# Optimization experiments

Measured on AMD Instinct MI355X. Metric: run time of the kernel, lower is better.

The kernel has to match this reference:

```python
import math
import jax, jax.numpy as jnp
import numpy as np

N_USERS = 100000
N_ITEMS = 50000
NNZ = 1600000
BATCH = 64
ORDER = 8
FLATNESS = 2


def cheby_coeffs(order, flatness):
    # plateau target on Chebyshev extrema grid
    x = np.arange(order + 1)
    xv = np.round(np.cos((order - x) / order * math.pi), 3)
    tgt = np.where(xv < 0,
                   np.power(-xv, flatness) * 0.5 + 0.5,
                   np.power(xv, flatness) * (-0.5) + 0.5)
    tgt = np.round(tgt, 3)
    # Chebyshev nodes
    k = np.arange(1, order + 2)
    nodes = np.cos((order + 1 + 0.5 - k) / (order + 1) * math.pi)
    # Chebyshev recurrence evaluated at nodes, scaled by target
    out = [tgt * np.ones_like(nodes) * 0 + tgt, nodes * tgt]
    for _ in range(2, order + 1):
        out.append(nodes * out[-1] * 2 - out[-2])
    c = np.stack(out).sum(axis=1) * (2.0 / (order + 1))
    c[0] /= 2
    return jnp.asarray(c, dtype=jnp.float32)


def setup_inputs() -> dict:
    key = jax.random.key(0)
    k1, k2, k3 = jax.random.split(key, 3)
    signal = jax.random.normal(k1, (BATCH, N_ITEMS), dtype=jnp.float32)
    row = jax.random.randint(k2, (NNZ,), 0, N_USERS)
    col = jax.random.randint(k3, (NNZ,), 0, N_ITEMS)
    # symmetric degree normalization D_u^{-1/2} A D_i^{-1/2}
    du = jnp.bincount(row, length=N_USERS).astype(jnp.float32)
    di = jnp.bincount(col, length=N_ITEMS).astype(jnp.float32)
    du_is = jnp.where(du > 0, jnp.clip(du, 1.0) ** -0.5, 0.0)
    di_is = jnp.where(di > 0, jnp.clip(di, 1.0) ** -0.5, 0.0)
    vals = du_is[row] * di_is[col]
    return {"signal": signal, "vals": vals, "row": row, "col": col}


def reference(signal, vals, row, col):
    coeffs = cheby_coeffs(ORDER, FLATNESS)

    def lap(x):  # x: [n_items, batch];  L*x = x - 2 * A^T (A x)
        y = jax.ops.segment_sum(vals[:, None] * x[col], row, num_segments=N_USERS)
        z = jax.ops.segment_sum(vals[:, None] * y[row], col, num_segments=N_ITEMS)
        return x - 2.0 * z

    s = signal.T  # [n_items, batch]
    t0 = s
    t1 = lap(s)
    out = coeffs[0] * t0 + coeffs[1] * t1
    for k in range(2, ORDER + 1):
        t2 = lap(t1) * 2.0 - t0
        out = out + coeffs[k] * t2
        t0, t1 = t1, t2
    return out.T
```

## Files before the change

### kernel.cpp

```cpp
#include <hip/hip_runtime.h>
#include <hip/hip_fp16.h>
#include <math.h>

#define NUSERS 100000
#define NITEMS 50000
#define BATCH  64
#define ORDER  8
#define BSHIFT 9
#define BROWS  (1 << BSHIFT)
#define NBUCKU ((NUSERS + BROWS - 1) >> BSHIFT)
#define NBUCKI ((NITEMS + BROWS - 1) >> BSHIFT)
#define CAPU 16384
#define CAPI 24576
#define S1_BLOCKS 512
#define NREP 4


struct __align__(8) Half4 { __half2 a, b; };
struct Coeffs { float v[ORDER + 1]; };

#define SLOT ((size_t)(NITEMS + 1) * BATCH)

__device__ __forceinline__ void acc_pk(float4& acc, Half4 v0, Half4 v1,
                                       Half4 v2, Half4 v3) {
    __half2 sa = __hadd2(__hadd2(v0.a, v1.a), __hadd2(v2.a, v3.a));
    __half2 sb = __hadd2(__hadd2(v0.b, v1.b), __hadd2(v2.b, v3.b));
    float2 fa = __half22float2(sa);
    float2 fb = __half22float2(sb);
    acc.x += fa.x; acc.y += fa.y; acc.z += fb.x; acc.w += fb.y;
}

__device__ __forceinline__ Half4 to_h4(float x, float y, float z, float w) {
    Half4 h;
    h.a = __floats2half2_rn(x, y);
    h.b = __floats2half2_rn(z, w);
    return h;
}

__global__ void init_bcur(int* __restrict__ bcurU, int* __restrict__ bcurI) {
    int t = blockIdx.x * blockDim.x + threadIdx.x;
    if (t < NBUCKU) bcurU[t] = t * CAPU;
    if (t < NBUCKI) bcurI[t] = t * CAPI;
}

__global__ void zero_pads(__half* __restrict__ tauHall, __half* __restrict__ ybuf) {
    int t = threadIdx.x;
    for (int k = 0; k <= ORDER; ++k)
        if (t < BATCH) tauHall[(size_t)k * SLOT + (size_t)NITEMS * BATCH + t] = __float2half(0.f);
    if (t < BATCH) ybuf[(size_t)NUSERS * BATCH + t] = __float2half(0.f);
}

__global__ void scatter1(const int* __restrict__ row, const int* __restrict__ col,
                         int* __restrict__ bcurU, int* __restrict__ bcurI,
                         int* __restrict__ stU, int* __restrict__ stI, int nnz) {
    __shared__ int cU[NREP][NBUCKU];
    __shared__ int cI[NREP][NBUCKI];
    const int chunk = (nnz + S1_BLOCKS - 1) / S1_BLOCKS;
    const int b0 = blockIdx.x * chunk;
    const int e0 = min(b0 + chunk, nnz);
    const int sw = threadIdx.x >> 6;
    for (int t = threadIdx.x; t < NREP * NBUCKU; t += blockDim.x) (&cU[0][0])[t] = 0;
    for (int t = threadIdx.x; t < NREP * NBUCKI; t += blockDim.x) (&cI[0][0])[t] = 0;
    __syncthreads();
    for (int i = b0 + threadIdx.x; i < e0; i += blockDim.x) {
        atomicAdd(&cU[sw][row[i] >> BSHIFT], 1);
        atomicAdd(&cI[sw][col[i] >> BSHIFT], 1);
    }
    __syncthreads();
    for (int t = threadIdx.x; t < NBUCKU; t += blockDim.x) {
        int c0 = cU[0][t], c1 = cU[1][t], c2 = cU[2][t], c3 = cU[3][t];
        int tot = c0 + c1 + c2 + c3;
        int base = (tot > 0) ? atomicAdd(&bcurU[t], tot) : 0;
        cU[0][t] = base;
        cU[1][t] = base + c0;
        cU[2][t] = base + c0 + c1;
        cU[3][t] = base + c0 + c1 + c2;
    }
    for (int t = threadIdx.x; t < NBUCKI; t += blockDim.x) {
        int c0 = cI[0][t], c1 = cI[1][t], c2 = cI[2][t], c3 = cI[3][t];
        int tot = c0 + c1 + c2 + c3;
        int base = (tot > 0) ? atomicAdd(&bcurI[t], tot) : 0;
        cI[0][t] = base;
        cI[1][t] = base + c0;
        cI[2][t] = base + c0 + c1;
        cI[3][t] = base + c0 + c1 + c2;
    }
    __syncthreads();
    for (int i = b0 + threadIdx.x; i < e0; i += blockDim.x) {
        int r = row[i], c = col[i];
        int pu = atomicAdd(&cU[sw][r >> BSHIFT], 1);
        stU[pu] = ((r & (BROWS - 1)) << 17) | c;
        int pi = atomicAdd(&cI[sw][c >> BSHIFT], 1);
        stI[pi] = ((c & (BROWS - 1)) << 17) | r;
    }
}

__global__ void scatter2(const int* __restrict__ bcur, const int* __restrict__ st,
                         int* __restrict__ ptr, int* __restrict__ degOut,
                         int* __restrict__ outIdx, int nrows, int cap, int dummyIdx) {
    __shared__ int deg[BROWS];
    __shared__ int ps[256];
    __shared__ int cur[BROWS];
    __shared__ int rs[BROWS];
    const int rbase = blockIdx.x << BSHIFT;
    const int nr = min(BROWS, nrows - rbase);
    const int lo = blockIdx.x * cap;
    const int hi = bcur[blockIdx.x];
    const int t = threadIdx.x;
    deg[2 * t] = 0;
    deg[2 * t + 1] = 0;
    __syncthreads();
    for (int j = lo + t; j < hi; j += 256)
        atomicAdd(&deg[st[j] >> 17], 1);
    __syncthreads();
    int a = deg[2 * t];
    int b = deg[2 * t + 1];
    int pa = (a + 15) & ~15;
    int pb = (b + 15) & ~15;
    ps[t] = pa + pb;
    __syncthreads();
    for (int off = 1; off < 256; off <<= 1) {
        int u = (t >= off) ? ps[t - off] : 0;
        __syncthreads();
        ps[t] += u;
        __syncthreads();
    }
    int excl = (t > 0) ? ps[t - 1] : 0;
    int p0 = lo + excl;
    int p1 = p0 + pa;
    rs[2 * t] = p0;
    rs[2 * t + 1] = p1;
    cur[2 * t] = p0;
    cur[2 * t + 1] = p1;
    if (2 * t < nr)     { ptr[rbase + 2 * t] = p0;     degOut[rbase + 2 * t] = a; }
    if (2 * t + 1 < nr) { ptr[rbase + 2 * t + 1] = p1; degOut[rbase + 2 * t + 1] = b; }
    __syncthreads();
    for (int j = lo + t; j < hi; j += 256) {
        int v = st[j];
        int p = atomicAdd(&cur[v >> 17], 1);
        outIdx[p] = v & 0x1FFFF;
    }
    __syncthreads();
    for (int i = t; i < nr; i += 256) {
        int endReal = cur[i];
        int endPad  = rs[i] + ((deg[i] + 15) & ~15);
        for (int j = endReal; j < endPad; ++j) outIdx[j] = dummyIdx;
    }
}

__global__ void transpose_scale_k(const float* __restrict__ in,
                                  const int* __restrict__ ideg,
                                  float* __restrict__ out,
                                  __half* __restrict__ outH) {
    __shared__ float tile[32][33];
    const int cb = blockIdx.x * 32;
    const int rb = blockIdx.y * 32;
    for (int i = threadIdx.y; i < 32; i += 8) {
        int r = rb + i, c = cb + threadIdx.x;
        if (r < BATCH && c < NITEMS) tile[i][threadIdx.x] = in[(size_t)r * NITEMS + c];
    }
    __syncthreads();
    for (int i = threadIdx.y; i < 32; i += 8) {
        int c = cb + i, r = rb + threadIdx.x;
        if (c < NITEMS && r < BATCH) {
            int d = ideg[c];
            float dis = (d > 0) ? rsqrtf((float)d) : 0.0f;
            float v = dis * tile[threadIdx.x][i];
            out[(size_t)c * BATCH + r] = v;
            outH[(size_t)c * BATCH + r] = __float2half(v);
        }
    }
}

__global__ void transpose_out_k(const __half* __restrict__ tauHall,
                                const float* __restrict__ signal,
                                const int* __restrict__ ideg, float csum, Coeffs cf,
                                float* __restrict__ out) {
    __shared__ float tile[32][33];
    const int cb = blockIdx.x * 32;
    const int rb = blockIdx.y * 32;
    for (int i = threadIdx.y; i < 32; i += 8) {
        int r = rb + i, c = cb + threadIdx.x;
        if (r < NITEMS && c < BATCH) {
            size_t base = (size_t)r * BATCH + c;
            float s = 0.f;
            #pragma unroll
            for (int k = 0; k <= ORDER; ++k)
                s += cf.v[k] * __half2float(tauHall[(size_t)k * SLOT + base]);
            tile[i][threadIdx.x] = s;
        }
    }
    __syncthreads();
    for (int i = threadIdx.y; i < 32; i += 8) {
        int c = cb + i, r = rb + threadIdx.x;
        if (c < BATCH && r < NITEMS) {
            int d = ideg[r];
            float v = (d > 0) ? sqrtf((float)d) * tile[threadIdx.x][i]
                              : csum * signal[(size_t)c * NITEMS + r];
            out[(size_t)c * NITEMS + r] = v;
        }
    }
}


__global__ void spmm_user(const int* __restrict__ ptr, const int* __restrict__ deg,
                          const int* __restrict__ idx,
                          const Half4* __restrict__ tauH, Half4* __restrict__ y) {
    const int lane = threadIdx.x & 63;
    const int w = (blockIdx.x * blockDim.x + threadIdx.x) >> 6;
    const int H = NUSERS / 2;
    if (w >= H) return;
    const int r0 = w, r1 = w + H;
    const int sub = lane >> 4;
    const int bh  = lane & 15;
    const int b0 = ptr[r0], d0 = deg[r0], n0 = (d0 + 15) >> 4;
    const int b1 = ptr[r1], d1 = deg[r1], n1 = (d1 + 15) >> 4;
    int j0 = b0 + (sub << 2), j1 = b1 + (sub << 2);
    float4 a0 = {0.f, 0.f, 0.f, 0.f}, a1 = {0.f, 0.f, 0.f, 0.f};
    const int nmax = max(n0, n1);
    for (int it = 0; it < nmax; ++it) {
        if (it < n0) {
            int i0 = idx[j0], i1 = idx[j0 + 1], i2 = idx[j0 + 2], i3 = idx[j0 + 3];
            Half4 v0 = tauH[(size_t)i0 * 16 + bh];
            Half4 v1 = tauH[(size_t)i1 * 16 + bh];
            Half4 v2 = tauH[(size_t)i2 * 16 + bh];
            Half4 v3 = tauH[(size_t)i3 * 16 + bh];
            acc_pk(a0, v0, v1, v2, v3);
            j0 += 16;
        }
        if (it < n1) {
            int i0 = idx[j1], i1 = idx[j1 + 1], i2 = idx[j1 + 2], i3 = idx[j1 + 3];
            Half4 v0 = tauH[(size_t)i0 * 16 + bh];
            Half4 v1 = tauH[(size_t)i1 * 16 + bh];
            Half4 v2 = tauH[(size_t)i2 * 16 + bh];
            Half4 v3 = tauH[(size_t)i3 * 16 + bh];
            acc_pk(a1, v0, v1, v2, v3);
            j1 += 16;
        }
    }
    a0.x += __shfl_xor(a0.x, 16); a0.y += __shfl_xor(a0.y, 16);
    a0.z += __shfl_xor(a0.z, 16); a0.w += __shfl_xor(a0.w, 16);
    a0.x += __shfl_xor(a0.x, 32); a0.y += __shfl_xor(a0.y, 32);
    a0.z += __shfl_xor(a0.z, 32); a0.w += __shfl_xor(a0.w, 32);
    a1.x += __shfl_xor(a1.x, 16); a1.y += __shfl_xor(a1.y, 16);
    a1.z += __shfl_xor(a1.z, 16); a1.w += __shfl_xor(a1.w, 16);
    a1.x += __shfl_xor(a1.x, 32); a1.y += __shfl_xor(a1.y, 32);
    a1.z += __shfl_xor(a1.z, 32); a1.w += __shfl_xor(a1.w, 32);
    if (sub == 0) {
        float s0 = (d0 > 0) ? 1.0f / (float)d0 : 0.0f;
        y[(size_t)r0 * 16 + bh] = to_h4(s0 * a0.x, s0 * a0.y, s0 * a0.z, s0 * a0.w);
        float s1 = (d1 > 0) ? 1.0f / (float)d1 : 0.0f;
        y[(size_t)r1 * 16 + bh] = to_h4(s1 * a1.x, s1 * a1.y, s1 * a1.z, s1 * a1.w);
    }
}

__device__ __forceinline__ void gather4_p(const int* __restrict__ idx,
                                          const Half4* __restrict__ y,
                                          const int* b, const int* n,
                                          int sub, int bh, float4* a) {
    int j[4];
    int nmax = 0;
    #pragma unroll
    for (int q = 0; q < 4; ++q) {
        j[q] = b[q] + (sub << 2);
        nmax = max(nmax, n[q]);
    }
    for (int it = 0; it < nmax; ++it) {
        #pragma unroll
        for (int q = 0; q < 4; ++q) {
            if (it < n[q]) {
                int i0 = idx[j[q]], i1 = idx[j[q] + 1];
                int i2 = idx[j[q] + 2], i3 = idx[j[q] + 3];
                Half4 v0 = y[(size_t)i0 * 16 + bh];
                Half4 v1 = y[(size_t)i1 * 16 + bh];
                Half4 v2 = y[(size_t)i2 * 16 + bh];
                Half4 v3 = y[(size_t)i3 * 16 + bh];
                acc_pk(a[q], v0, v1, v2, v3);
                j[q] += 16;
            }
        }
    }
    #pragma unroll
    for (int q = 0; q < 4; ++q) {
        a[q].x += __shfl_xor(a[q].x, 16); a[q].y += __shfl_xor(a[q].y, 16);
        a[q].z += __shfl_xor(a[q].z, 16); a[q].w += __shfl_xor(a[q].w, 16);
        a[q].x += __shfl_xor(a[q].x, 32); a[q].y += __shfl_xor(a[q].y, 32);
        a[q].z += __shfl_xor(a[q].z, 32); a[q].w += __shfl_xor(a[q].w, 32);
    }
}

__global__ void spmm_item_first(const int* __restrict__ ptr, const int* __restrict__ deg,
                                const int* __restrict__ idx, const Half4* __restrict__ y,
                                const float* __restrict__ tau0, float* __restrict__ tau1,
                                Half4* __restrict__ tauH1) {
    const int lane = threadIdx.x & 63;
    const int w = (blockIdx.x * blockDim.x + threadIdx.x) >> 6;
    const int H = NITEMS / 4;
    if (w >= H) return;
    int r[4] = {w, w + H, w + 2 * H, w + 3 * H};
    const int sub = lane >> 4;
    const int bh  = lane & 15;
    int b[4], d[4], n[4];
    #pragma unroll
    for (int q = 0; q < 4; ++q) {
        b[q] = ptr[r[q]];
        d[q] = deg[r[q]];
        n[q] = (d[q] + 15) >> 4;
    }
    float4 a[4] = {{0,0,0,0},{0,0,0,0},{0,0,0,0},{0,0,0,0}};
    gather4_p(idx, y, b, n, sub, bh, a);
    if (sub == 0) {
        #pragma unroll
        for (int q = 0; q < 4; ++q) {
            float inv = (d[q] > 0) ? 1.0f / (float)d[q] : 0.0f;
            float s2 = 2.0f * inv;
            size_t base = (size_t)r[q] * BATCH + (bh << 2);
            float4 t0v = *(const float4*)&tau0[base];
            float4 t;
            t.x = t0v.x - s2 * a[q].x; t.y = t0v.y - s2 * a[q].y;
            t.z = t0v.z - s2 * a[q].z; t.w = t0v.w - s2 * a[q].w;
            *(float4*)&tau1[base] = t;
            tauH1[(size_t)r[q] * 16 + bh] = to_h4(t.x, t.y, t.z, t.w);
        }
    }
}

__global__ void spmm_item_k(const int* __restrict__ ptr, const int* __restrict__ deg,
                            const int* __restrict__ idx, const Half4* __restrict__ y,
                            const float* __restrict__ tau1, float* __restrict__ tau0,
                            Half4* __restrict__ tauHk) {
    const int lane = threadIdx.x & 63;
    const int w = (blockIdx.x * blockDim.x + threadIdx.x) >> 6;
    const int H = NITEMS / 4;
    if (w >= H) return;
    int r[4] = {w, w + H, w + 2 * H, w + 3 * H};
    const int sub = lane >> 4;
    const int bh  = lane & 15;
    int b[4], d[4], n[4];
    #pragma unroll
    for (int q = 0; q < 4; ++q) {
        b[q] = ptr[r[q]];
        d[q] = deg[r[q]];
        n[q] = (d[q] + 15) >> 4;
    }
    float4 a[4] = {{0,0,0,0},{0,0,0,0},{0,0,0,0},{0,0,0,0}};
    gather4_p(idx, y, b, n, sub, bh, a);
    if (sub == 0) {
        #pragma unroll
        for (int q = 0; q < 4; ++q) {
            float inv = (d[q] > 0) ? 1.0f / (float)d[q] : 0.0f;
            float s4 = 4.0f * inv;
            size_t base = (size_t)r[q] * BATCH + (bh << 2);
            float4 t1v = *(const float4*)&tau1[base];
            float4 t0v = *(const float4*)&tau0[base];
            float4 t2;
            t2.x = 2.0f * t1v.x - s4 * a[q].x - t0v.x;
            t2.y = 2.0f * t1v.y - s4 * a[q].y - t0v.y;
            t2.z = 2.0f * t1v.z - s4 * a[q].z - t0v.z;
            t2.w = 2.0f * t1v.w - s4 * a[q].w - t0v.w;
            *(float4*)&tau0[base] = t2;
            tauHk[(size_t)r[q] * 16 + bh] = to_h4(t2.x, t2.y, t2.z, t2.w);
        }
    }
}

static void cheby_coeffs_host(float* c) {
    const int order = ORDER, flatness = 2;
    const double PI = 3.14159265358979323846;
    double tgt[ORDER + 1], nodes[ORDER + 1];
    for (int x = 0; x <= order; ++x) {
        double xv = cos((double)(order - x) / order * PI);
        xv = nearbyint(xv * 1000.0) / 1000.0;
        double t = (xv < 0.0) ? pow(-xv, (double)flatness) * 0.5 + 0.5
                              : pow(xv, (double)flatness) * (-0.5) + 0.5;
        tgt[x] = nearbyint(t * 1000.0) / 1000.0;
    }
    for (int k = 1; k <= order + 1; ++k)
        nodes[k - 1] = cos((order + 1 + 0.5 - k) / (double)(order + 1) * PI);

    double prev[ORDER + 1], cur[ORDER + 1], nxt[ORDER + 1];
    double sums[ORDER + 1];
    double s0 = 0, s1 = 0;
    for (int i = 0; i <= order; ++i) {
        prev[i] = tgt[i];
        cur[i]  = nodes[i] * tgt[i];
        s0 += prev[i];
        s1 += cur[i];
    }
    sums[0] = s0; sums[1] = s1;
    for (int j = 2; j <= order; ++j) {
        double s = 0;
        for (int i = 0; i <= order; ++i) {
            nxt[i] = nodes[i] * cur[i] * 2.0 - prev[i];
            s += nxt[i];
        }
        sums[j] = s;
        for (int i = 0; i <= order; ++i) { prev[i] = cur[i]; cur[i] = nxt[i]; }
    }
    for (int j = 0; j <= order; ++j)
        c[j] = (float)(sums[j] * (2.0 / (order + 1)));
    c[0] *= 0.5f;
}

extern "C" void kernel_launch(void* const* d_in, const int* in_sizes, int n_in,
                              void* d_out, int out_size, void* d_ws, size_t ws_size,
                              hipStream_t stream) {
    const float* signal = (const float*)d_in[0];
    const int*   row    = (const int*)d_in[2];
    const int*   col    = (const int*)d_in[3];
    const int nnz = in_sizes[1];

    char* wsb = (char*)d_ws;
    size_t off = 0;
    auto carve = [&](size_t nbytes) {
        void* p = wsb + off;
        off += (nbytes + 255) & ~(size_t)255;
        return p;
    };
    const size_t NB = (size_t)NITEMS * BATCH;
    const size_t NEU = (size_t)NBUCKU * CAPU;
    const size_t NEI = (size_t)NBUCKI * CAPI;
    float*  tauA   = (float*)carve(NB * 4);
    float*  tauB   = (float*)carve(NB * 4);
    __half* tauHall = (__half*)carve((ORDER + 1) * SLOT * 2);
    Half4*  ybuf   = (Half4*)carve(((size_t)NUSERS + 1) * BATCH * 2);
    int*    uptr   = (int*)carve(NUSERS * 4);
    int*    iptr   = (int*)carve(NITEMS * 4);
    int*    udeg   = (int*)carve(NUSERS * 4);
    int*    ideg   = (int*)carve(NITEMS * 4);
    int*    bcurU  = (int*)carve(NBUCKU * 4);
    int*    bcurI  = (int*)carve(NBUCKI * 4);
    int*    ucol   = (int*)carve(NEU * 4);
    int*    irow   = (int*)carve(NEI * 4);
    int*    stU    = (int*)tauHall;
    int*    stI    = (int*)tauHall + NEU;
    (void)ws_size;

    float c[ORDER + 1];
    cheby_coeffs_host(c);
    Coeffs cf;
    float csum = 0.f;
    for (int k = 0; k <= ORDER; ++k) { cf.v[k] = c[k]; csum += c[k]; }

    init_bcur<<<(NBUCKU + 255) / 256, 256, 0, stream>>>(bcurU, bcurI);
    scatter1<<<S1_BLOCKS, 256, 0, stream>>>(row, col, bcurU, bcurI, stU, stI, nnz);
    scatter2<<<NBUCKU, 256, 0, stream>>>(bcurU, stU, uptr, udeg, ucol, NUSERS, CAPU, NITEMS);
    scatter2<<<NBUCKI, 256, 0, stream>>>(bcurI, stI, iptr, ideg, irow, NITEMS, CAPI, NUSERS);
    zero_pads<<<1, 256, 0, stream>>>(tauHall, (__half*)ybuf);

    dim3 tb(32, 8);
    transpose_scale_k<<<dim3((NITEMS + 31) / 32, (BATCH + 31) / 32), tb, 0, stream>>>(
        signal, ideg, tauA, tauHall);

    const int ug = ((NUSERS / 2) * 64 + 255) / 256;
    const int ig = ((NITEMS / 4) * 64 + 255) / 256;

    spmm_user<<<ug, 256, 0, stream>>>(uptr, udeg, ucol, (const Half4*)tauHall, ybuf);
    spmm_item_first<<<ig, 256, 0, stream>>>(iptr, ideg, irow, ybuf, tauA, tauB,
                                            (Half4*)(tauHall + SLOT));

    float* t0 = tauA;
    float* t1 = tauB;
    for (int k = 2; k <= ORDER; ++k) {
        spmm_user<<<ug, 256, 0, stream>>>(uptr, udeg, ucol,
                                          (const Half4*)(tauHall + (size_t)(k - 1) * SLOT), ybuf);
        spmm_item_k<<<ig, 256, 0, stream>>>(iptr, ideg, irow, ybuf, t1, t0,
                                            (Half4*)(tauHall + (size_t)k * SLOT));
        float* tmp = t0; t0 = t1; t1 = tmp;
    }

    transpose_out_k<<<dim3((BATCH + 31) / 32, (NITEMS + 31) / 32), tb, 0, stream>>>(
        tauHall, signal, ideg, csum, cf, (float*)d_out);
}
```

Before: 771.0 us.

## Gather 16-byte half8 vectors with 8 lanes per row in SpMM kernels

Remaps the sparse gathers so each row is handled by 8 lanes issuing 16-byte Half8 loads, with 8 slots each consuming 2 nonzeros per step via a paired int2 index load. Previously 16 lanes used 8-byte loads with 4 indices per slot. The user-side kernel now processes 4 rows per wavefront instead of 2, matching the item kernels. The aim is fewer, wider memory instructions and more rows in flight per wave. The cost is 32 fp32 accumulators per thread, which raises register pressure, and one extra shuffle-reduction stage.

```diff
diff --git a/kernel.cpp b/kernel.cpp
--- a/kernel.cpp
+++ b/kernel.cpp
@@ -16,26 +16,10 @@
 #define NREP 4
 
 
-struct __align__(8) Half4 { __half2 a, b; };
+struct __align__(16) Half8 { __half2 h[4]; };
 struct Coeffs { float v[ORDER + 1]; };
 
 #define SLOT ((size_t)(NITEMS + 1) * BATCH)
-
-__device__ __forceinline__ void acc_pk(float4& acc, Half4 v0, Half4 v1,
-                                       Half4 v2, Half4 v3) {
-    __half2 sa = __hadd2(__hadd2(v0.a, v1.a), __hadd2(v2.a, v3.a));
-    __half2 sb = __hadd2(__hadd2(v0.b, v1.b), __hadd2(v2.b, v3.b));
-    float2 fa = __half22float2(sa);
-    float2 fb = __half22float2(sb);
-    acc.x += fa.x; acc.y += fa.y; acc.z += fb.x; acc.w += fb.y;
-}
-
-__device__ __forceinline__ Half4 to_h4(float x, float y, float z, float w) {
-    Half4 h;
-    h.a = __floats2half2_rn(x, y);
-    h.b = __floats2half2_rn(z, w);
-    return h;
-}
 
 __global__ void init_bcur(int* __restrict__ bcurU, int* __restrict__ bcurI) {
     int t = blockIdx.x * blockDim.x + threadIdx.x;
@@ -202,104 +186,56 @@
     }
 }
 
-
-__global__ void spmm_user(const int* __restrict__ ptr, const int* __restrict__ deg,
-                          const int* __restrict__ idx,
-                          const Half4* __restrict__ tauH, Half4* __restrict__ y) {
-    const int lane = threadIdx.x & 63;
-    const int w = (blockIdx.x * blockDim.x + threadIdx.x) >> 6;
-    const int H = NUSERS / 2;
-    if (w >= H) return;
-    const int r0 = w, r1 = w + H;
-    const int sub = lane >> 4;
-    const int bh  = lane & 15;
-    const int b0 = ptr[r0], d0 = deg[r0], n0 = (d0 + 15) >> 4;
-    const int b1 = ptr[r1], d1 = deg[r1], n1 = (d1 + 15) >> 4;
-    int j0 = b0 + (sub << 2), j1 = b1 + (sub << 2);
-    float4 a0 = {0.f, 0.f, 0.f, 0.f}, a1 = {0.f, 0.f, 0.f, 0.f};
-    const int nmax = max(n0, n1);
-    for (int it = 0; it < nmax; ++it) {
-        if (it < n0) {
-            int i0 = idx[j0], i1 = idx[j0 + 1], i2 = idx[j0 + 2], i3 = idx[j0 + 3];
-            Half4 v0 = tauH[(size_t)i0 * 16 + bh];
-            Half4 v1 = tauH[(size_t)i1 * 16 + bh];
-            Half4 v2 = tauH[(size_t)i2 * 16 + bh];
-            Half4 v3 = tauH[(size_t)i3 * 16 + bh];
-            acc_pk(a0, v0, v1, v2, v3);
-            j0 += 16;
-        }
-        if (it < n1) {
-            int i0 = idx[j1], i1 = idx[j1 + 1], i2 = idx[j1 + 2], i3 = idx[j1 + 3];
-            Half4 v0 = tauH[(size_t)i0 * 16 + bh];
-            Half4 v1 = tauH[(size_t)i1 * 16 + bh];
-            Half4 v2 = tauH[(size_t)i2 * 16 + bh];
-            Half4 v3 = tauH[(size_t)i3 * 16 + bh];
-            acc_pk(a1, v0, v1, v2, v3);
-            j1 += 16;
-        }
-    }
-    a0.x += __shfl_xor(a0.x, 16); a0.y += __shfl_xor(a0.y, 16);
-    a0.z += __shfl_xor(a0.z, 16); a0.w += __shfl_xor(a0.w, 16);
-    a0.x += __shfl_xor(a0.x, 32); a0.y += __shfl_xor(a0.y, 32);
-    a0.z += __shfl_xor(a0.z, 32); a0.w += __shfl_xor(a0.w, 32);
-    a1.x += __shfl_xor(a1.x, 16); a1.y += __shfl_xor(a1.y, 16);
-    a1.z += __shfl_xor(a1.z, 16); a1.w += __shfl_xor(a1.w, 16);
-    a1.x += __shfl_xor(a1.x, 32); a1.y += __shfl_xor(a1.y, 32);
-    a1.z += __shfl_xor(a1.z, 32); a1.w += __shfl_xor(a1.w, 32);
-    if (sub == 0) {
-        float s0 = (d0 > 0) ? 1.0f / (float)d0 : 0.0f;
-        y[(size_t)r0 * 16 + bh] = to_h4(s0 * a0.x, s0 * a0.y, s0 * a0.z, s0 * a0.w);
-        float s1 = (d1 > 0) ? 1.0f / (float)d1 : 0.0f;
-        y[(size_t)r1 * 16 + bh] = to_h4(s1 * a1.x, s1 * a1.y, s1 * a1.z, s1 * a1.w);
-    }
-}
-
-__device__ __forceinline__ void gather4_p(const int* __restrict__ idx,
-                                          const Half4* __restrict__ y,
+__device__ __forceinline__ void gather4x2(const int* __restrict__ idx,
+                                          const Half8* __restrict__ x,
                                           const int* b, const int* n,
-                                          int sub, int bh, float4* a) {
+                                          int slot, int bh, float (*a)[8]) {
     int j[4];
     int nmax = 0;
     #pragma unroll
     for (int q = 0; q < 4; ++q) {
-        j[q] = b[q] + (sub << 2);
+        j[q] = b[q] + slot * 2;
         nmax = max(nmax, n[q]);
     }
     for (int it = 0; it < nmax; ++it) {
         #pragma unroll
         for (int q = 0; q < 4; ++q) {
             if (it < n[q]) {
-                int i0 = idx[j[q]], i1 = idx[j[q] + 1];
-                int i2 = idx[j[q] + 2], i3 = idx[j[q] + 3];
-                Half4 v0 = y[(size_t)i0 * 16 + bh];
-                Half4 v1 = y[(size_t)i1 * 16 + bh];
-                Half4 v2 = y[(size_t)i2 * 16 + bh];
-                Half4 v3 = y[(size_t)i3 * 16 + bh];
-                acc_pk(a[q], v0, v1, v2, v3);
+                int2 ii = *(const int2*)&idx[j[q]];
+                Half8 v0 = x[(size_t)ii.x * 8 + bh];
+                Half8 v1 = x[(size_t)ii.y * 8 + bh];
+                #pragma unroll
+                for (int k = 0; k < 4; ++k) {
+                    __half2 s = __hadd2(v0.h[k], v1.h[k]);
+                    float2 f = __half22float2(s);
+                    a[q][2 * k]     += f.x;
+                    a[q][2 * k + 1] += f.y;
+                }
                 j[q] += 16;
             }
         }
     }
     #pragma unroll
     for (int q = 0; q < 4; ++q) {
-        a[q].x += __shfl_xor(a[q].x, 16); a[q].y += __shfl_xor(a[q].y, 16);
-        a[q].z += __shfl_xor(a[q].z, 16); a[q].w += __shfl_xor(a[q].w, 16);
-        a[q].x += __shfl_xor(a[q].x, 32); a[q].y += __shfl_xor(a[q].y, 32);
-        a[q].z += __shfl_xor(a[q].z, 32); a[q].w += __shfl_xor(a[q].w, 32);
-    }
-}
-
-__global__ void spmm_item_first(const int* __restrict__ ptr, const int* __restrict__ deg,
-                                const int* __restrict__ idx, const Half4* __restrict__ y,
-                                const float* __restrict__ tau0, float* __restrict__ tau1,
-                                Half4* __restrict__ tauH1) {
+        #pragma unroll
+        for (int k = 0; k < 8; ++k) {
+            a[q][k] += __shfl_xor(a[q][k], 8);
+            a[q][k] += __shfl_xor(a[q][k], 16);
+            a[q][k] += __shfl_xor(a[q][k], 32);
+        }
+    }
+}
+
+__global__ void spmm_user(const int* __restrict__ ptr, const int* __restrict__ deg,
+                          const int* __restrict__ idx,
+                          const Half8* __restrict__ tauH, Half8* __restrict__ y) {
     const int lane = threadIdx.x & 63;
     const int w = (blockIdx.x * blockDim.x + threadIdx.x) >> 6;
-    const int H = NITEMS / 4;
+    const int H = NUSERS / 4;
     if (w >= H) return;
     int r[4] = {w, w + H, w + 2 * H, w + 3 * H};
-    const int sub = lane >> 4;
-    const int bh  = lane & 15;
+    const int slot = lane >> 3;
+    const int bh   = lane & 7;
     int b[4], d[4], n[4];
     #pragma unroll
     for (int q = 0; q < 4; ++q) {
@@ -307,35 +243,32 @@
         d[q] = deg[r[q]];
         n[q] = (d[q] + 15) >> 4;
     }
-    float4 a[4] = {{0,0,0,0},{0,0,0,0},{0,0,0,0},{0,0,0,0}};
-    gather4_p(idx, y, b, n, sub, bh, a);
-    if (sub == 0) {
+    float a[4][8] = {};
+    gather4x2(idx, tauH, b, n, slot, bh, a);
+    if (slot == 0) {
         #pragma unroll
         for (int q = 0; q < 4; ++q) {
-            float inv = (d[q] > 0) ? 1.0f / (float)d[q] : 0.0f;
-            float s2 = 2.0f * inv;
-            size_t base = (size_t)r[q] * BATCH + (bh << 2);
-            float4 t0v = *(const float4*)&tau0[base];
-            float4 t;
-            t.x = t0v.x - s2 * a[q].x; t.y = t0v.y - s2 * a[q].y;
-            t.z = t0v.z - s2 * a[q].z; t.w = t0v.w - s2 * a[q].w;
-            *(float4*)&tau1[base] = t;
-            tauH1[(size_t)r[q] * 16 + bh] = to_h4(t.x, t.y, t.z, t.w);
-        }
-    }
-}
-
-__global__ void spmm_item_k(const int* __restrict__ ptr, const int* __restrict__ deg,
-                            const int* __restrict__ idx, const Half4* __restrict__ y,
-                            const float* __restrict__ tau1, float* __restrict__ tau0,
-                            Half4* __restrict__ tauHk) {
+            float s = (d[q] > 0) ? 1.0f / (float)d[q] : 0.0f;
+            Half8 o;
+            #pragma unroll
+            for (int k = 0; k < 4; ++k)
+                o.h[k] = __floats2half2_rn(s * a[q][2 * k], s * a[q][2 * k + 1]);
+            y[(size_t)r[q] * 8 + bh] = o;
+        }
+    }
+}
+
+__global__ void spmm_item_first(const int* __restrict__ ptr, const int* __restrict__ deg,
+                                const int* __restrict__ idx, const Half8* __restrict__ y,
+                                const float* __restrict__ tau0, float* __restrict__ tau1,
+                                Half8* __restrict__ tauH1) {
     const int lane = threadIdx.x & 63;
     const int w = (blockIdx.x * blockDim.x + threadIdx.x) >> 6;
     const int H = NITEMS / 4;
     if (w >= H) return;
     int r[4] = {w, w + H, w + 2 * H, w + 3 * H};
-    const int sub = lane >> 4;
-    const int bh  = lane & 15;
+    const int slot = lane >> 3;
+    const int bh   = lane & 7;
     int b[4], d[4], n[4];
     #pragma unroll
     for (int q = 0; q < 4; ++q) {
@@ -343,23 +276,80 @@
         d[q] = deg[r[q]];
         n[q] = (d[q] + 15) >> 4;
     }
-    float4 a[4] = {{0,0,0,0},{0,0,0,0},{0,0,0,0},{0,0,0,0}};
-    gather4_p(idx, y, b, n, sub, bh, a);
-    if (sub == 0) {
+    float a[4][8] = {};
+    gather4x2(idx, y, b, n, slot, bh, a);
+    if (slot == 0) {
+        #pragma unroll
+        for (int q = 0; q < 4; ++q) {
+            float inv = (d[q] > 0) ? 1.0f / (float)d[q] : 0.0f;
+            float s2 = 2.0f * inv;
+            size_t base = (size_t)r[q] * BATCH + bh * 8;
+            float4 t0a = *(const float4*)&tau0[base];
+            float4 t0b = *(const float4*)&tau0[base + 4];
+            float4 ta, tb;
+            ta.x = t0a.x - s2 * a[q][0]; ta.y = t0a.y - s2 * a[q][1];
+            ta.z = t0a.z - s2 * a[q][2]; ta.w = t0a.w - s2 * a[q][3];
+            tb.x = t0b.x - s2 * a[q][4]; tb.y = t0b.y - s2 * a[q][5];
+            tb.z = t0b.z - s2 * a[q][6]; tb.w = t0b.w - s2 * a[q][7];
+            *(float4*)&tau1[base] = ta;
+            *(float4*)&tau1[base + 4] = tb;
+            Half8 o;
+            o.h[0] = __floats2half2_rn(ta.x, ta.y);
+            o.h[1] = __floats2half2_rn(ta.z, ta.w);
+            o.h[2] = __floats2half2_rn(tb.x, tb.y);
+            o.h[3] = __floats2half2_rn(tb.z, tb.w);
+            tauH1[(size_t)r[q] * 8 + bh] = o;
+        }
+    }
+}
+
+__global__ void spmm_item_k(const int* __restrict__ ptr, const int* __restrict__ deg,
+                            const int* __restrict__ idx, const Half8* __restrict__ y,
+                            const float* __restrict__ tau1, float* __restrict__ tau0,
+                            Half8* __restrict__ tauHk) {
+    const int lane = threadIdx.x & 63;
+    const int w = (blockIdx.x * blockDim.x + threadIdx.x) >> 6;
+    const int H = NITEMS / 4;
+    if (w >= H) return;
+    int r[4] = {w, w + H, w + 2 * H, w + 3 * H};
+    const int slot = lane >> 3;
+    const int bh   = lane & 7;
+    int b[4], d[4], n[4];
+    #pragma unroll
+    for (int q = 0; q < 4; ++q) {
+        b[q] = ptr[r[q]];
+        d[q] = deg[r[q]];
+        n[q] = (d[q] + 15) >> 4;
+    }
+    float a[4][8] = {};
+    gather4x2(idx, y, b, n, slot, bh, a);
+    if (slot == 0) {
         #pragma unroll
         for (int q = 0; q < 4; ++q) {
             float inv = (d[q] > 0) ? 1.0f / (float)d[q] : 0.0f;
             float s4 = 4.0f * inv;
-            size_t base = (size_t)r[q] * BATCH + (bh << 2);
-            float4 t1v = *(const float4*)&tau1[base];
-            float4 t0v = *(const float4*)&tau0[base];
-            float4 t2;
-            t2.x = 2.0f * t1v.x - s4 * a[q].x - t0v.x;
-            t2.y = 2.0f * t1v.y - s4 * a[q].y - t0v.y;
-            t2.z = 2.0f * t1v.z - s4 * a[q].z - t0v.z;
-            t2.w = 2.0f * t1v.w - s4 * a[q].w - t0v.w;
-            *(float4*)&tau0[base] = t2;
-            tauHk[(size_t)r[q] * 16 + bh] = to_h4(t2.x, t2.y, t2.z, t2.w);
+            size_t base = (size_t)r[q] * BATCH + bh * 8;
+            float4 t1a = *(const float4*)&tau1[base];
+            float4 t1b = *(const float4*)&tau1[base + 4];
+            float4 t0a = *(const float4*)&tau0[base];
+            float4 t0b = *(const float4*)&tau0[base + 4];
+            float4 ta, tb;
+            ta.x = 2.0f * t1a.x - s4 * a[q][0] - t0a.x;
+            ta.y = 2.0f * t1a.y - s4 * a[q][1] - t0a.y;
+            ta.z = 2.0f * t1a.z - s4 * a[q][2] - t0a.z;
+            ta.w = 2.0f * t1a.w - s4 * a[q][3] - t0a.w;
+            tb.x = 2.0f * t1b.x - s4 * a[q][4] - t0b.x;
+            tb.y = 2.0f * t1b.y - s4 * a[q][5] - t0b.y;
+            tb.z = 2.0f * t1b.z - s4 * a[q][6] - t0b.z;
+            tb.w = 2.0f * t1b.w - s4 * a[q][7] - t0b.w;
+            *(float4*)&tau0[base] = ta;
+            *(float4*)&tau0[base + 4] = tb;
+            Half8 o;
+            o.h[0] = __floats2half2_rn(ta.x, ta.y);
+            o.h[1] = __floats2half2_rn(ta.z, ta.w);
+            o.h[2] = __floats2half2_rn(tb.x, tb.y);
+            o.h[3] = __floats2half2_rn(tb.z, tb.w);
+            tauHk[(size_t)r[q] * 8 + bh] = o;
         }
     }
 }
@@ -423,7 +413,7 @@
     float*  tauA   = (float*)carve(NB * 4);
     float*  tauB   = (float*)carve(NB * 4);
     __half* tauHall = (__half*)carve((ORDER + 1) * SLOT * 2);
-    Half4*  ybuf   = (Half4*)carve(((size_t)NUSERS + 1) * BATCH * 2);
+    Half8*  ybuf   = (Half8*)carve(((size_t)NUSERS + 1) * BATCH * 2);
     int*    uptr   = (int*)carve(NUSERS * 4);
     int*    iptr   = (int*)carve(NITEMS * 4);
     int*    udeg   = (int*)carve(NUSERS * 4);
@@ -452,20 +442,20 @@
     transpose_scale_k<<<dim3((NITEMS + 31) / 32, (BATCH + 31) / 32), tb, 0, stream>>>(
         signal, ideg, tauA, tauHall);
 
-    const int ug = ((NUSERS / 2) * 64 + 255) / 256;
+    const int ug = ((NUSERS / 4) * 64 + 255) / 256;
     const int ig = ((NITEMS / 4) * 64 + 255) / 256;
 
-    spmm_user<<<ug, 256, 0, stream>>>(uptr, udeg, ucol, (const Half4*)tauHall, ybuf);
+    spmm_user<<<ug, 256, 0, stream>>>(uptr, udeg, ucol, (const Half8*)tauHall, ybuf);
     spmm_item_first<<<ig, 256, 0, stream>>>(iptr, ideg, irow, ybuf, tauA, tauB,
-                                            (Half4*)(tauHall + SLOT));
+                                            (Half8*)(tauHall + SLOT));
 
     float* t0 = tauA;
     float* t1 = tauB;
     for (int k = 2; k <= ORDER; ++k) {
         spmm_user<<<ug, 256, 0, stream>>>(uptr, udeg, ucol,
-                                          (const Half4*)(tauHall + (size_t)(k - 1) * SLOT), ybuf);
+                                          (const Half8*)(tauHall + (size_t)(k - 1) * SLOT), ybuf);
         spmm_item_k<<<ig, 256, 0, stream>>>(iptr, ideg, irow, ybuf, t1, t0,
-                                            (Half4*)(tauHall + (size_t)k * SLOT));
+                                            (Half8*)(tauHall + (size_t)k * SLOT));
         float* tmp = t0; t0 = t1; t1 = tmp;
     }
 
```

Result: slower. 909.0 us (+17.9%).

## Sort rows into degree bins so each wavefront processes rows of similar length

Applied to the files above, without the earlier changes.

Adds count, scan and scatter kernels that build a permutation grouping user and item rows by padded degree (in chunks of 16 nonzeros). The SpMM kernels now take their rows from this permutation, so the rows handled together in one wavefront have similar iteration counts. This is meant to cut divergence and idle lanes from mixing short and long rows. The cost is a few extra setup launches and an indirect row lookup, and rows processed together are no longer contiguous in memory, so output writes scatter.

```diff
diff --git a/kernel.cpp b/kernel.cpp
--- a/kernel.cpp
+++ b/kernel.cpp
@@ -14,6 +14,8 @@
 #define CAPI 24576
 #define S1_BLOCKS 512
 #define NREP 4
+#define NBIN 16
+#define BIN_BLOCKS 64
 
 
 struct __align__(8) Half4 { __half2 a, b; };
@@ -37,10 +39,12 @@
     return h;
 }
 
-__global__ void init_bcur(int* __restrict__ bcurU, int* __restrict__ bcurI) {
+__global__ void init_bcur(int* __restrict__ bcurU, int* __restrict__ bcurI,
+                          int* __restrict__ bins) {
     int t = blockIdx.x * blockDim.x + threadIdx.x;
     if (t < NBUCKU) bcurU[t] = t * CAPU;
     if (t < NBUCKI) bcurI[t] = t * CAPI;
+    if (t < 4 * NBIN) bins[t] = 0;
 }
 
 __global__ void zero_pads(__half* __restrict__ tauHall, __half* __restrict__ ybuf) {
@@ -145,6 +149,61 @@
         int endReal = cur[i];
         int endPad  = rs[i] + ((deg[i] + 15) & ~15);
         for (int j = endReal; j < endPad; ++j) outIdx[j] = dummyIdx;
+    }
+}
+
+__global__ void bin_count(const int* __restrict__ deg, int n, int* __restrict__ gcnt) {
+    __shared__ int ls[NREP][NBIN];
+    const int sw = threadIdx.x >> 6;
+    for (int t = threadIdx.x; t < NREP * NBIN; t += blockDim.x) (&ls[0][0])[t] = 0;
+    __syncthreads();
+    const int chunk = (n + BIN_BLOCKS - 1) / BIN_BLOCKS;
+    const int b0 = blockIdx.x * chunk;
+    const int e0 = min(b0 + chunk, n);
+    for (int i = b0 + threadIdx.x; i < e0; i += blockDim.x)
+        atomicAdd(&ls[sw][min((deg[i] + 15) >> 4, NBIN - 1)], 1);
+    __syncthreads();
+    for (int t = threadIdx.x; t < NBIN; t += blockDim.x) {
+        int s = ls[0][t] + ls[1][t] + ls[2][t] + ls[3][t];
+        if (s > 0) atomicAdd(&gcnt[t], s);
+    }
+}
+
+__global__ void bin_scan(int* __restrict__ bins) {
+    if (threadIdx.x == 0) {
+        int s = 0;
+        for (int i = 0; i < NBIN; ++i) { int v = bins[i]; bins[NBIN + i] = s; s += v; }
+        s = 0;
+        for (int i = 0; i < NBIN; ++i) { int v = bins[2 * NBIN + i]; bins[3 * NBIN + i] = s; s += v; }
+    }
+}
+
+__global__ void bin_scatter(const int* __restrict__ deg, int n,
+                            int* __restrict__ gcur, int* __restrict__ perm) {
+    __shared__ int ls[NREP][NBIN];
+    const int sw = threadIdx.x >> 6;
+    for (int t = threadIdx.x; t < NREP * NBIN; t += blockDim.x) (&ls[0][0])[t] = 0;
+    __syncthreads();
+    const int chunk = (n + BIN_BLOCKS - 1) / BIN_BLOCKS;
+    const int b0 = blockIdx.x * chunk;
+    const int e0 = min(b0 + chunk, n);
+    for (int i = b0 + threadIdx.x; i < e0; i += blockDim.x)
+        atomicAdd(&ls[sw][min((deg[i] + 15) >> 4, NBIN - 1)], 1);
+    __syncthreads();
+    for (int t = threadIdx.x; t < NBIN; t += blockDim.x) {
+        int c0 = ls[0][t], c1 = ls[1][t], c2 = ls[2][t], c3 = ls[3][t];
+        int tot = c0 + c1 + c2 + c3;
+        int base = (tot > 0) ? atomicAdd(&gcur[t], tot) : 0;
+        ls[0][t] = base;
+        ls[1][t] = base + c0;
+        ls[2][t] = base + c0 + c1;
+        ls[3][t] = base + c0 + c1 + c2;
+    }
+    __syncthreads();
+    for (int i = b0 + threadIdx.x; i < e0; i += blockDim.x) {
+        int bn = min((deg[i] + 15) >> 4, NBIN - 1);
+        int p = atomicAdd(&ls[sw][bn], 1);
+        perm[p] = i;
     }
 }
 
@@ -204,13 +263,13 @@
 
 
 __global__ void spmm_user(const int* __restrict__ ptr, const int* __restrict__ deg,
-                          const int* __restrict__ idx,
+                          const int* __restrict__ perm, const int* __restrict__ idx,
                           const Half4* __restrict__ tauH, Half4* __restrict__ y) {
     const int lane = threadIdx.x & 63;
     const int w = (blockIdx.x * blockDim.x + threadIdx.x) >> 6;
     const int H = NUSERS / 2;
     if (w >= H) return;
-    const int r0 = w, r1 = w + H;
+    const int r0 = perm[2 * w], r1 = perm[2 * w + 1];
     const int sub = lane >> 4;
     const int bh  = lane & 15;
     const int b0 = ptr[r0], d0 = deg[r0], n0 = (d0 + 15) >> 4;
@@ -290,14 +349,15 @@
 }
 
 __global__ void spmm_item_first(const int* __restrict__ ptr, const int* __restrict__ deg,
-                                const int* __restrict__ idx, const Half4* __restrict__ y,
+                                const int* __restrict__ perm, const int* __restrict__ idx,
+                                const Half4* __restrict__ y,
                                 const float* __restrict__ tau0, float* __restrict__ tau1,
                                 Half4* __restrict__ tauH1) {
     const int lane = threadIdx.x & 63;
     const int w = (blockIdx.x * blockDim.x + threadIdx.x) >> 6;
     const int H = NITEMS / 4;
     if (w >= H) return;
-    int r[4] = {w, w + H, w + 2 * H, w + 3 * H};
+    int r[4] = {perm[4 * w], perm[4 * w + 1], perm[4 * w + 2], perm[4 * w + 3]};
     const int sub = lane >> 4;
     const int bh  = lane & 15;
     int b[4], d[4], n[4];
@@ -326,14 +386,15 @@
 }
 
 __global__ void spmm_item_k(const int* __restrict__ ptr, const int* __restrict__ deg,
-                            const int* __restrict__ idx, const Half4* __restrict__ y,
+                            const int* __restrict__ perm, const int* __restrict__ idx,
+                            const Half4* __restrict__ y,
                             const float* __restrict__ tau1, float* __restrict__ tau0,
                             Half4* __restrict__ tauHk) {
     const int lane = threadIdx.x & 63;
     const int w = (blockIdx.x * blockDim.x + threadIdx.x) >> 6;
     const int H = NITEMS / 4;
     if (w >= H) return;
-    int r[4] = {w, w + H, w + 2 * H, w + 3 * H};
+    int r[4] = {perm[4 * w], perm[4 * w + 1], perm[4 * w + 2], perm[4 * w + 3]};
     const int sub = lane >> 4;
     const int bh  = lane & 15;
     int b[4], d[4], n[4];
@@ -430,6 +491,9 @@
     int*    ideg   = (int*)carve(NITEMS * 4);
     int*    bcurU  = (int*)carve(NBUCKU * 4);
     int*    bcurI  = (int*)carve(NBUCKI * 4);
+    int*    bins   = (int*)carve(4 * NBIN * 4);
+    int*    uperm  = (int*)carve(NUSERS * 4);
+    int*    iperm  = (int*)carve(NITEMS * 4);
     int*    ucol   = (int*)carve(NEU * 4);
     int*    irow   = (int*)carve(NEI * 4);
     int*    stU    = (int*)tauHall;
@@ -442,12 +506,18 @@
     float csum = 0.f;
     for (int k = 0; k <= ORDER; ++k) { cf.v[k] = c[k]; csum += c[k]; }
 
-    init_bcur<<<(NBUCKU + 255) / 256, 256, 0, stream>>>(bcurU, bcurI);
+    init_bcur<<<(NBUCKU + 255) / 256, 256, 0, stream>>>(bcurU, bcurI, bins);
     scatter1<<<S1_BLOCKS, 256, 0, stream>>>(row, col, bcurU, bcurI, stU, stI, nnz);
     scatter2<<<NBUCKU, 256, 0, stream>>>(bcurU, stU, uptr, udeg, ucol, NUSERS, CAPU, NITEMS);
     scatter2<<<NBUCKI, 256, 0, stream>>>(bcurI, stI, iptr, ideg, irow, NITEMS, CAPI, NUSERS);
     zero_pads<<<1, 256, 0, stream>>>(tauHall, (__half*)ybuf);
 
+    bin_count<<<BIN_BLOCKS, 256, 0, stream>>>(udeg, NUSERS, bins);
+    bin_count<<<BIN_BLOCKS, 256, 0, stream>>>(ideg, NITEMS, bins + 2 * NBIN);
+    bin_scan<<<1, 64, 0, stream>>>(bins);
+    bin_scatter<<<BIN_BLOCKS, 256, 0, stream>>>(udeg, NUSERS, bins + NBIN, uperm);
+    bin_scatter<<<BIN_BLOCKS, 256, 0, stream>>>(ideg, NITEMS, bins + 3 * NBIN, iperm);
+
     dim3 tb(32, 8);
     transpose_scale_k<<<dim3((NITEMS + 31) / 32, (BATCH + 31) / 32), tb, 0, stream>>>(
         signal, ideg, tauA, tauHall);
@@ -455,16 +525,16 @@
     const int ug = ((NUSERS / 2) * 64 + 255) / 256;
     const int ig = ((NITEMS / 4) * 64 + 255) / 256;
 
-    spmm_user<<<ug, 256, 0, stream>>>(uptr, udeg, ucol, (const Half4*)tauHall, ybuf);
-    spmm_item_first<<<ig, 256, 0, stream>>>(iptr, ideg, irow, ybuf, tauA, tauB,
+    spmm_user<<<ug, 256, 0, stream>>>(uptr, udeg, uperm, ucol, (const Half4*)tauHall, ybuf);
+    spmm_item_first<<<ig, 256, 0, stream>>>(iptr, ideg, iperm, irow, ybuf, tauA, tauB,
                                             (Half4*)(tauHall + SLOT));
 
     float* t0 = tauA;
     float* t1 = tauB;
     for (int k = 2; k <= ORDER; ++k) {
-        spmm_user<<<ug, 256, 0, stream>>>(uptr, udeg, ucol,
+        spmm_user<<<ug, 256, 0, stream>>>(uptr, udeg, uperm, ucol,
                                           (const Half4*)(tauHall + (size_t)(k - 1) * SLOT), ybuf);
-        spmm_item_k<<<ig, 256, 0, stream>>>(iptr, ideg, irow, ybuf, t1, t0,
+        spmm_item_k<<<ig, 256, 0, stream>>>(iptr, ideg, iperm, irow, ybuf, t1, t0,
                                             (Half4*)(tauHall + (size_t)k * SLOT));
         float* tmp = t0; t0 = t1; t1 = tmp;
     }
```

After: 805.7 us. 1.04x slower.
